# Kernel optimization log

Hardware: AMD Instinct MI355X
Metric: run time of the kernel (lower is better)

Reference implementation:

```python
import jax, jax.numpy as jnp
import numpy as np

B, S, D, H = 2, 2048, 2048, 16
HD = D // H  # 128


def setup_inputs() -> dict:
    key = jax.random.key(0)
    ks = jax.random.split(key, 5)
    x = jax.random.normal(ks[0], (B, S, D), dtype=jnp.float32)
    scale = 1.0 / np.sqrt(D)
    wq = jax.random.normal(ks[1], (D, D), dtype=jnp.float32) * scale
    wk = jax.random.normal(ks[2], (D, D), dtype=jnp.float32) * scale
    wv = jax.random.normal(ks[3], (D, D), dtype=jnp.float32) * scale
    wo = jax.random.normal(ks[4], (D, D), dtype=jnp.float32) * scale
    # RoPE frequencies: theta = 10000, freqs_cis[t, j] = exp(i * t / theta^(2j/HD))
    inv_freq = 1.0 / (10000.0 ** (jnp.arange(0, HD, 2, dtype=jnp.float32) / HD))  # [HD/2]
    t = jnp.arange(S, dtype=jnp.float32)
    ang = jnp.outer(t, inv_freq)  # [S, HD/2]
    freqs_cos = jnp.cos(ang)
    freqs_sin = jnp.sin(ang)
    # Additive causal mask [S, S]
    neg = jnp.float32(-1e9)
    mask = jnp.triu(jnp.full((S, S), neg, dtype=jnp.float32), k=1)
    return {"x": x, "wq": wq, "wk": wk, "wv": wv, "wo": wo,
            "freqs_cos": freqs_cos, "freqs_sin": freqs_sin,
            "mask": mask, "start_pos": 0}


def _rope(t, cos, sin):
    # t: [B, S, H, HD]; cos/sin: [S, HD/2] broadcast as [1, S, 1, HD/2]
    tr = t.reshape(t.shape[:-1] + (HD // 2, 2))
    xr, xi = tr[..., 0], tr[..., 1]
    c = cos[None, :, None, :]
    s = sin[None, :, None, :]
    out_r = xr * c - xi * s
    out_i = xr * s + xi * c
    return jnp.stack([out_r, out_i], axis=-1).reshape(t.shape)


def reference(x, wq, wk, wv, wo, freqs_cos, freqs_sin, mask, start_pos):
    bsz, seqlen, _ = x.shape
    # nn.Linear: y = x @ W.T
    xq = jnp.einsum('bsd,ed->bse', x, wq).reshape(bsz, seqlen, H, HD)
    xk = jnp.einsum('bsd,ed->bse', x, wk).reshape(bsz, seqlen, H, HD)
    xv = jnp.einsum('bsd,ed->bse', x, wv).reshape(bsz, seqlen, H, HD)
    xq = _rope(xq, freqs_cos, freqs_sin)
    xk = _rope(xk, freqs_cos, freqs_sin)
    # [B, H, S, HD]
    xq = xq.transpose(0, 2, 1, 3)
    xk = xk.transpose(0, 2, 1, 3)
    xv = xv.transpose(0, 2, 1, 3)
    scores = jnp.einsum('bhqd,bhkd->bhqk', xq, xk) / jnp.sqrt(jnp.float32(HD))
    scores = scores + mask[None, None, :, :]
    probs = jax.nn.softmax(scores.astype(jnp.float32), axis=-1).astype(xq.dtype)
    out = jnp.einsum('bhqk,bhkd->bhqd', probs, xv)
    out = out.transpose(0, 2, 1, 3).reshape(bsz, seqlen, H * HD)
    return jnp.einsum('bse,de->bsd', out, wo)
```

## Files before the change

### kernel.cpp

```cpp
#include <hip/hip_runtime.h>


#define SQ 2048
#define DQ 2048
#define HQ 16
#define HDQ 128

typedef short bf16x8 __attribute__((ext_vector_type(8)));
typedef short bf16x4 __attribute__((ext_vector_type(4)));
typedef float f32x4 __attribute__((ext_vector_type(4)));

#define WAITVM4 asm volatile("s_waitcnt vmcnt(4)" ::: "memory")
#define WAITVM3 asm volatile("s_waitcnt vmcnt(3)" ::: "memory")
#define WAITVM2 asm volatile("s_waitcnt vmcnt(2)" ::: "memory")
#define WAITVM0 asm volatile("s_waitcnt vmcnt(0)" ::: "memory")

__device__ __forceinline__ short f2bf(float f) {
  union { float f; unsigned u; } v; v.f = f;
  unsigned r = (v.u + 0x7FFFu + ((v.u >> 16) & 1u)) >> 16;
  return (short)r;
}
__device__ __forceinline__ float bf2f(short b) {
  union { unsigned u; float f; } v; v.u = ((unsigned)(unsigned short)b) << 16;
  return v.f;
}
__device__ __forceinline__ void gload_lds16(const void* g, void* l) {
  __builtin_amdgcn_global_load_lds(
      (const __attribute__((address_space(1))) void*)g,
      (__attribute__((address_space(3))) void*)l, 16, 0, 0);
}

__global__ void cvt_kernel(const float* __restrict__ in, short* __restrict__ out, int nvec) {
  int i = blockIdx.x * blockDim.x + threadIdx.x;
  if (i >= nvec) return;
  const f32x4* p = (const f32x4*)in + (size_t)i * 2;
  f32x4 a = p[0], b = p[1];
  bf16x8 o;
  o[0] = f2bf(a[0]); o[1] = f2bf(a[1]); o[2] = f2bf(a[2]); o[3] = f2bf(a[3]);
  o[4] = f2bf(b[0]); o[5] = f2bf(b[1]); o[6] = f2bf(b[2]); o[7] = f2bf(b[3]);
  *((bf16x8*)out + i) = o;
}

__global__ void rope_kernel(short* __restrict__ t, const float* __restrict__ cosT,
                            const float* __restrict__ sinT, float scale, int nvec) {
  int i = blockIdx.x * blockDim.x + threadIdx.x;
  if (i >= nvec) return;
  size_t off = (size_t)i * 8;
  int hd0 = (int)(off & 127);
  int s = (int)((off >> 7) & 2047);
  bf16x8 v = *((const bf16x8*)(t + off));
  f32x4 c  = *(const f32x4*)(cosT + (size_t)s * 64 + (hd0 >> 1));
  f32x4 sn = *(const f32x4*)(sinT + (size_t)s * 64 + (hd0 >> 1));
  bf16x8 o;
#pragma unroll
  for (int p = 0; p < 4; ++p) {
    float xr = bf2f(v[2 * p]), xi = bf2f(v[2 * p + 1]);
    o[2 * p]     = f2bf((xr * c[p] - xi * sn[p]) * scale);
    o[2 * p + 1] = f2bf((xr * sn[p] + xi * c[p]) * scale);
  }
  *((bf16x8*)(t + off)) = o;
}

__global__ void vtrans_kernel(const short* __restrict__ vb, short* __restrict__ vtb) {
  __shared__ __align__(16) short tile[64][72];
  int bh = blockIdx.z, s0 = blockIdx.y * 64, d0 = blockIdx.x * 64;
  int tid = threadIdx.x;
#pragma unroll
  for (int it = 0; it < 2; ++it) {
    int vi = it * 256 + tid;
    int r = vi >> 3, c8 = (vi & 7) * 8;
    bf16x8 v = *(const bf16x8*)&vb[((size_t)bh * SQ + s0 + r) * HDQ + d0 + c8];
    *(bf16x8*)&tile[r][c8] = v;
  }
  __syncthreads();
#pragma unroll
  for (int it = 0; it < 2; ++it) {
    int vi = it * 256 + tid;
    int d = vi >> 3, s8 = (vi & 7) * 8;
    bf16x8 o;
#pragma unroll
    for (int j = 0; j < 8; ++j) o[j] = tile[s8 + j][d];
    *(bf16x8*)&vtb[((size_t)bh * HDQ + d0 + d) * SQ + s0 + s8] = o;
  }
}

template <int BN, int MODE>
__global__ __launch_bounds__(512, 4) void gemmT(const short* __restrict__ A,
                                                const short* __restrict__ W,
                                                short* __restrict__ oQ, short* __restrict__ oK,
                                                short* __restrict__ oV, float* __restrict__ oF) {
  constexpr int NFR = BN / 64;
  constexpr int NIB = BN / 16;
  constexpr int NBX = (MODE == 0) ? (6144 / BN) : (2048 / BN);
  __shared__ __align__(16) short As[3][128 * 32];
  __shared__ __align__(16) short Bs[3][BN * 32];
  const int K = DQ;
  const int NT = K / 32;
  int nwg = gridDim.x, cpx = nwg >> 3;
  int swz = (blockIdx.x & 7) * cpx + (blockIdx.x >> 3);
  int bx = swz % NBX, by = swz / NBX;
  int m0 = by * 128, n0 = bx * BN;
  int tid = threadIdx.x, wid = tid >> 6, lane = tid & 63;
  int wr = wid >> 2, wc = wid & 3;
  f32x4 acc[4][NFR] = {};

  auto stageA = [&](int kt, int buf) {
    int g = wid * 64 + lane;
    int r = g >> 2, q = g & 3;
    gload_lds16(A + (size_t)(m0 + r) * K + kt * 32 + ((q ^ (((r >> 3) & 1) << 1)) * 8),
                &As[buf][wid * 512]);
  };
  auto stageB = [&](int kt, int buf) {
#pragma unroll
    for (int i = wid; i < NIB; i += 8) {
      int g = i * 64 + lane;
      int r = g >> 2, q = g & 3;
      gload_lds16(W + (size_t)(n0 + r) * K + kt * 32 + ((q ^ (((r >> 3) & 1) << 1)) * 8),
                  &Bs[buf][i * 512]);
    }
  };

  stageA(0, 0); stageB(0, 0);
  stageA(1, 1); stageB(1, 1);
  if (BN == 192 && wid < 4) { WAITVM3; } else { WAITVM2; }
  __builtin_amdgcn_s_barrier();

  int cc = (lane >> 4) * 8;
  int cur = 0, nbuf = 2;
#pragma unroll 1
  for (int t = 0; t < NT; ++t) {
    bool st = (t + 2) < NT;
    bf16x8 bfr[NFR], af[4];
#pragma unroll
    for (int nf = 0; nf < NFR; ++nf) {
      int br = wc * (BN / 4) + nf * 16 + (lane & 15);
      bfr[nf] = *(const bf16x8*)&Bs[cur][br * 32 + (cc ^ (((br >> 3) & 1) << 4))];
    }
#pragma unroll
    for (int i = 0; i < 4; ++i) {
      int fr = wr * 64 + i * 16 + (lane & 15);
      af[i] = *(const bf16x8*)&As[cur][fr * 32 + (cc ^ (((fr >> 3) & 1) << 4))];
    }
    if (st) { stageA(t + 2, nbuf); stageB(t + 2, nbuf); }
    __builtin_amdgcn_s_setprio(1);
#pragma unroll
    for (int i = 0; i < 4; ++i)
#pragma unroll
      for (int nf = 0; nf < NFR; ++nf)
        acc[i][nf] = __builtin_amdgcn_mfma_f32_16x16x32_bf16(af[i], bfr[nf], acc[i][nf], 0, 0, 0);
    __builtin_amdgcn_s_setprio(0);
    if (st) {
      if (BN == 192 && wid < 4) { WAITVM3; } else { WAITVM2; }
    } else {
      WAITVM0;
    }
    __builtin_amdgcn_s_barrier();
    cur = (cur == 2) ? 0 : cur + 1;
    nbuf = (nbuf == 2) ? 0 : nbuf + 1;
  }
#pragma unroll
  for (int mf = 0; mf < 4; ++mf) {
    int mb = m0 + wr * 64 + mf * 16 + (lane >> 4) * 4;
#pragma unroll
    for (int nf = 0; nf < NFR; ++nf) {
      int n_lin = n0 + wc * (BN / 4) + nf * 16 + (lane & 15);
#pragma unroll
      for (int j = 0; j < 4; ++j) {
        int m = mb + j;
        float v = acc[mf][nf][j];
        if (MODE == 0) {
          int zsel = n_lin >> 11, col = n_lin & 2047;
          short* oT = (zsel == 0) ? oQ : (zsel == 1) ? oK : oV;
          int b = m >> 11, s = m & 2047, h = col >> 7, hd = col & 127;
          oT[(((size_t)(b * HQ + h)) * SQ + s) * HDQ + hd] = f2bf(v);
        } else {
          oF[(size_t)m * DQ + n_lin] = v;
        }
      }
    }
  }
}

__device__ __forceinline__ void stage_kv32(const short* kbase, const short* vbase, int k0,
                                           short* KsB, short* VtB, int w, int lane) {
#pragma unroll
  for (int i = 0; i < 2; ++i) {
    int c = i * 4 + w;
    int ch = c * 64 + lane;
    int r = ch >> 4, c8 = (ch & 15) * 8;
    gload_lds16(kbase + (size_t)(k0 + r) * HDQ + (c8 ^ ((r & 7) << 3)), KsB + c * 512);
    int d = ch >> 2, k8 = (ch & 3) * 8;
    gload_lds16(vbase + (size_t)d * SQ + k0 + (k8 ^ (((d >> 1) & 3) << 3)), VtB + c * 512);
  }
}

__global__ __launch_bounds__(256, 4) void flash_kernel(const short* __restrict__ qb,
                                                       const short* __restrict__ kb,
                                                       const short* __restrict__ vtb,
                                                       short* __restrict__ ab) {
  __shared__ __align__(16) short Ks[2][32 * 128];
  __shared__ __align__(16) short Vt[2][128 * 32];
  __shared__ __align__(16) short Pl[4][16 * 32];
  int x = blockIdx.x, bh = blockIdx.y;
  int qt = (bh & 8) ? (31 - x) : x;
  int q0 = qt * 64;
  int tid = threadIdx.x, w = tid >> 6, lane = tid & 63;
  int g = lane >> 4, qcol = lane & 15;
  int qw0 = q0 + w * 16;
  const short* qbase = qb + (size_t)bh * SQ * HDQ;
  const short* kbase = kb + (size_t)bh * SQ * HDQ;
  const short* vbase = vtb + (size_t)bh * HDQ * SQ;
  int b = bh >> 4, h = bh & 15;

  bf16x8 qf[4];
#pragma unroll
  for (int ccq = 0; ccq < 4; ++ccq)
    qf[ccq] = *(const bf16x8*)&qbase[(size_t)(qw0 + qcol) * HDQ + ccq * 32 + g * 8];

  f32x4 oacc[8] = {};
  float m_st = -1e30f, l_st = 0.f;
  int nt = 2 * qt + 2;
  stage_kv32(kbase, vbase, 0, Ks[0], Vt[0], w, lane);
#pragma unroll 1
  for (int t = 0; t < nt; ++t) {
    int cur = t & 1;
    int k0 = t * 32;
    __builtin_amdgcn_s_barrier();
    if (t + 1 < nt) {
      stage_kv32(kbase, vbase, (t + 1) * 32, Ks[cur ^ 1], Vt[cur ^ 1], w, lane);
      WAITVM4;
    } else {
      WAITVM0;
    }
    __builtin_amdgcn_s_barrier();
    if (k0 > qw0 + 15) continue;
    f32x4 sacc[2] = {};
    __builtin_amdgcn_s_setprio(1);
#pragma unroll
    for (int nf = 0; nf < 2; ++nf) {
      int rk = nf * 16 + qcol;
#pragma unroll
      for (int ccq = 0; ccq < 4; ++ccq) {
        int ck = ccq * 32 + g * 8;
        bf16x8 kf = *(const bf16x8*)&Ks[cur][rk * 128 + (ck ^ ((rk & 7) << 3))];
        sacc[nf] = __builtin_amdgcn_mfma_f32_16x16x32_bf16(kf, qf[ccq], sacc[nf], 0, 0, 0);
      }
    }
    __builtin_amdgcn_s_setprio(0);
    int q = qw0 + qcol;
    if (k0 + 31 > qw0) {
#pragma unroll
      for (int nf = 0; nf < 2; ++nf)
#pragma unroll
        for (int j = 0; j < 4; ++j) {
          int k = k0 + nf * 16 + g * 4 + j;
          if (k > q) sacc[nf][j] = -1e9f;
        }
    }
    float mt = fmaxf(fmaxf(fmaxf(sacc[0][0], sacc[0][1]), fmaxf(sacc[0][2], sacc[0][3])),
                     fmaxf(fmaxf(sacc[1][0], sacc[1][1]), fmaxf(sacc[1][2], sacc[1][3])));
    mt = fmaxf(mt, __shfl_xor(mt, 16));
    mt = fmaxf(mt, __shfl_xor(mt, 32));
    float mn = fmaxf(m_st, mt);
    float al = exp2f(m_st - mn);
    float p0[4], p1[4];
    float ls = 0.f;
#pragma unroll
    for (int j = 0; j < 4; ++j) { p0[j] = exp2f(sacc[0][j] - mn); ls += p0[j]; }
#pragma unroll
    for (int j = 0; j < 4; ++j) { p1[j] = exp2f(sacc[1][j] - mn); ls += p1[j]; }
    l_st = l_st * al + ls;
    m_st = mn;
    int sw = (qcol & 3) * 8;
    {
      bf16x4 pk;
      pk[0] = f2bf(p0[0]); pk[1] = f2bf(p0[1]); pk[2] = f2bf(p0[2]); pk[3] = f2bf(p0[3]);
      *(bf16x4*)&Pl[w][qcol * 32 + ((g * 4) ^ sw)] = pk;
      pk[0] = f2bf(p1[0]); pk[1] = f2bf(p1[1]); pk[2] = f2bf(p1[2]); pk[3] = f2bf(p1[3]);
      *(bf16x4*)&Pl[w][qcol * 32 + ((16 + g * 4) ^ sw)] = pk;
    }
    f32x4 alv;
    alv[0] = __shfl(al, g * 4 + 0);
    alv[1] = __shfl(al, g * 4 + 1);
    alv[2] = __shfl(al, g * 4 + 2);
    alv[3] = __shfl(al, g * 4 + 3);
#pragma unroll
    for (int df = 0; df < 8; ++df) oacc[df] *= alv;
    bf16x8 pf = *(const bf16x8*)&Pl[w][qcol * 32 + ((g * 8) ^ sw)];
    __builtin_amdgcn_s_setprio(1);
#pragma unroll
    for (int df = 0; df < 8; ++df) {
      int rd = df * 16 + qcol;
      bf16x8 vf = *(const bf16x8*)&Vt[cur][rd * 32 + ((g * 8) ^ (((rd >> 1) & 3) << 3))];
      oacc[df] = __builtin_amdgcn_mfma_f32_16x16x32_bf16(pf, vf, oacc[df], 0, 0, 0);
    }
    __builtin_amdgcn_s_setprio(0);
  }
  l_st += __shfl_xor(l_st, 16);
  l_st += __shfl_xor(l_st, 32);
  float inv = 1.0f / l_st;
  f32x4 invv;
  invv[0] = __shfl(inv, g * 4 + 0);
  invv[1] = __shfl(inv, g * 4 + 1);
  invv[2] = __shfl(inv, g * 4 + 2);
  invv[3] = __shfl(inv, g * 4 + 3);
#pragma unroll
  for (int df = 0; df < 8; ++df)
#pragma unroll
    for (int j = 0; j < 4; ++j) {
      int qq = qw0 + g * 4 + j;
      int dd = df * 16 + qcol;
      ab[((size_t)b * SQ + qq) * DQ + h * HDQ + dd] = f2bf(oacc[df][j] * invv[j]);
    }
}

extern "C" void kernel_launch(void* const* d_in, const int* in_sizes, int n_in,
                              void* d_out, int out_size, void* d_ws, size_t ws_size,
                              hipStream_t stream) {
  (void)in_sizes; (void)n_in; (void)out_size; (void)ws_size;
  const float* x  = (const float*)d_in[0];
  const float* wq = (const float*)d_in[1];
  const float* wk = (const float*)d_in[2];
  const float* wv = (const float*)d_in[3];
  const float* wo = (const float*)d_in[4];
  const float* fc = (const float*)d_in[5];
  const float* fs = (const float*)d_in[6];
  float* out = (float*)d_out;

  short* xb  = (short*)d_ws;
  short* wqb = xb + (size_t)8388608;
  short* wkb = wqb + (size_t)4194304;
  short* wvb = wkb + (size_t)4194304;
  short* wob = wvb + (size_t)4194304;
  short* qb  = wob + (size_t)4194304;
  short* kb  = qb + (size_t)8388608;
  short* ab  = kb + (size_t)8388608;
  short* vb  = (short*)d_out;
  short* vtb = vb + (size_t)8388608;

  cvt_kernel<<<4096, 256, 0, stream>>>(x, xb, 1048576);
  cvt_kernel<<<2048, 256, 0, stream>>>(wq, wqb, 524288);
  cvt_kernel<<<2048, 256, 0, stream>>>(wk, wkb, 524288);
  cvt_kernel<<<2048, 256, 0, stream>>>(wv, wvb, 524288);
  cvt_kernel<<<2048, 256, 0, stream>>>(wo, wob, 524288);

  gemmT<192, 0><<<dim3(1024), 512, 0, stream>>>(xb, wqb, qb, kb, vb, nullptr);

  rope_kernel<<<4096, 256, 0, stream>>>(qb, fc, fs, 0.12751744779976827f, 1048576);
  rope_kernel<<<4096, 256, 0, stream>>>(kb, fc, fs, 1.0f, 1048576);

  vtrans_kernel<<<dim3(2, 32, 32), 256, 0, stream>>>(vb, vtb);

  flash_kernel<<<dim3(32, 32), 256, 0, stream>>>(qb, kb, vtb, ab);

  gemmT<128, 1><<<dim3(512), 512, 0, stream>>>(ab, wob, nullptr, nullptr, nullptr, out);
}
```

Measured before the change: 293.9 us.

## Fuse RoPE and V transpose into QKV GEMM epilogue, merge conversion kernels

```diff
diff --git a/kernel.cpp b/kernel.cpp
--- a/kernel.cpp
+++ b/kernel.cpp
@@ -11,7 +11,6 @@
 typedef float f32x4 __attribute__((ext_vector_type(4)));
 
 #define WAITVM4 asm volatile("s_waitcnt vmcnt(4)" ::: "memory")
-#define WAITVM3 asm volatile("s_waitcnt vmcnt(3)" ::: "memory")
 #define WAITVM2 asm volatile("s_waitcnt vmcnt(2)" ::: "memory")
 #define WAITVM0 asm volatile("s_waitcnt vmcnt(0)" ::: "memory")
 
@@ -30,65 +29,39 @@
       (__attribute__((address_space(3))) void*)l, 16, 0, 0);
 }
 
-__global__ void cvt_kernel(const float* __restrict__ in, short* __restrict__ out, int nvec) {
-  int i = blockIdx.x * blockDim.x + threadIdx.x;
-  if (i >= nvec) return;
-  const f32x4* p = (const f32x4*)in + (size_t)i * 2;
+__global__ void cvt5_kernel(const float* __restrict__ x, const float* __restrict__ wq,
+                            const float* __restrict__ wk, const float* __restrict__ wv,
+                            const float* __restrict__ wo, short* __restrict__ xb,
+                            short* __restrict__ wqb, short* __restrict__ wkb,
+                            short* __restrict__ wvb, short* __restrict__ wob) {
+  int bi = blockIdx.x;
+  const float* src;
+  short* dst;
+  int off;
+  if (bi < 4096) {
+    src = x; dst = xb; off = bi;
+  } else {
+    int t = bi - 4096, wsel = t >> 11;
+    off = t & 2047;
+    src = (wsel == 0) ? wq : (wsel == 1) ? wk : (wsel == 2) ? wv : wo;
+    dst = (wsel == 0) ? wqb : (wsel == 1) ? wkb : (wsel == 2) ? wvb : wob;
+  }
+  int i = off * 256 + threadIdx.x;
+  const f32x4* p = (const f32x4*)src + (size_t)i * 2;
   f32x4 a = p[0], b = p[1];
   bf16x8 o;
   o[0] = f2bf(a[0]); o[1] = f2bf(a[1]); o[2] = f2bf(a[2]); o[3] = f2bf(a[3]);
   o[4] = f2bf(b[0]); o[5] = f2bf(b[1]); o[6] = f2bf(b[2]); o[7] = f2bf(b[3]);
-  *((bf16x8*)out + i) = o;
-}
-
-__global__ void rope_kernel(short* __restrict__ t, const float* __restrict__ cosT,
-                            const float* __restrict__ sinT, float scale, int nvec) {
-  int i = blockIdx.x * blockDim.x + threadIdx.x;
-  if (i >= nvec) return;
-  size_t off = (size_t)i * 8;
-  int hd0 = (int)(off & 127);
-  int s = (int)((off >> 7) & 2047);
-  bf16x8 v = *((const bf16x8*)(t + off));
-  f32x4 c  = *(const f32x4*)(cosT + (size_t)s * 64 + (hd0 >> 1));
-  f32x4 sn = *(const f32x4*)(sinT + (size_t)s * 64 + (hd0 >> 1));
-  bf16x8 o;
-#pragma unroll
-  for (int p = 0; p < 4; ++p) {
-    float xr = bf2f(v[2 * p]), xi = bf2f(v[2 * p + 1]);
-    o[2 * p]     = f2bf((xr * c[p] - xi * sn[p]) * scale);
-    o[2 * p + 1] = f2bf((xr * sn[p] + xi * c[p]) * scale);
-  }
-  *((bf16x8*)(t + off)) = o;
-}
-
-__global__ void vtrans_kernel(const short* __restrict__ vb, short* __restrict__ vtb) {
-  __shared__ __align__(16) short tile[64][72];
-  int bh = blockIdx.z, s0 = blockIdx.y * 64, d0 = blockIdx.x * 64;
-  int tid = threadIdx.x;
-#pragma unroll
-  for (int it = 0; it < 2; ++it) {
-    int vi = it * 256 + tid;
-    int r = vi >> 3, c8 = (vi & 7) * 8;
-    bf16x8 v = *(const bf16x8*)&vb[((size_t)bh * SQ + s0 + r) * HDQ + d0 + c8];
-    *(bf16x8*)&tile[r][c8] = v;
-  }
-  __syncthreads();
-#pragma unroll
-  for (int it = 0; it < 2; ++it) {
-    int vi = it * 256 + tid;
-    int d = vi >> 3, s8 = (vi & 7) * 8;
-    bf16x8 o;
-#pragma unroll
-    for (int j = 0; j < 8; ++j) o[j] = tile[s8 + j][d];
-    *(bf16x8*)&vtb[((size_t)bh * HDQ + d0 + d) * SQ + s0 + s8] = o;
-  }
+  *((bf16x8*)dst + i) = o;
 }
 
 template <int BN, int MODE>
 __global__ __launch_bounds__(512, 4) void gemmT(const short* __restrict__ A,
                                                 const short* __restrict__ W,
                                                 short* __restrict__ oQ, short* __restrict__ oK,
-                                                short* __restrict__ oV, float* __restrict__ oF) {
+                                                short* __restrict__ oV, float* __restrict__ oF,
+                                                const float* __restrict__ cosT,
+                                                const float* __restrict__ sinT) {
   constexpr int NFR = BN / 64;
   constexpr int NIB = BN / 16;
   constexpr int NBX = (MODE == 0) ? (6144 / BN) : (2048 / BN);
@@ -122,7 +95,7 @@
 
   stageA(0, 0); stageB(0, 0);
   stageA(1, 1); stageB(1, 1);
-  if (BN == 192 && wid < 4) { WAITVM3; } else { WAITVM2; }
+  WAITVM2;
   __builtin_amdgcn_s_barrier();
 
   int cc = (lane >> 4) * 8;
@@ -149,11 +122,7 @@
       for (int nf = 0; nf < NFR; ++nf)
         acc[i][nf] = __builtin_amdgcn_mfma_f32_16x16x32_bf16(af[i], bfr[nf], acc[i][nf], 0, 0, 0);
     __builtin_amdgcn_s_setprio(0);
-    if (st) {
-      if (BN == 192 && wid < 4) { WAITVM3; } else { WAITVM2; }
-    } else {
-      WAITVM0;
-    }
+    if (st) { WAITVM2; } else { WAITVM0; }
     __builtin_amdgcn_s_barrier();
     cur = (cur == 2) ? 0 : cur + 1;
     nbuf = (nbuf == 2) ? 0 : nbuf + 1;
@@ -164,17 +133,36 @@
 #pragma unroll
     for (int nf = 0; nf < NFR; ++nf) {
       int n_lin = n0 + wc * (BN / 4) + nf * 16 + (lane & 15);
-#pragma unroll
-      for (int j = 0; j < 4; ++j) {
-        int m = mb + j;
-        float v = acc[mf][nf][j];
-        if (MODE == 0) {
-          int zsel = n_lin >> 11, col = n_lin & 2047;
-          short* oT = (zsel == 0) ? oQ : (zsel == 1) ? oK : oV;
-          int b = m >> 11, s = m & 2047, h = col >> 7, hd = col & 127;
-          oT[(((size_t)(b * HQ + h)) * SQ + s) * HDQ + hd] = f2bf(v);
-        } else {
-          oF[(size_t)m * DQ + n_lin] = v;
+      if (MODE == 1) {
+#pragma unroll
+        for (int j = 0; j < 4; ++j)
+          oF[(size_t)(mb + j) * DQ + n_lin] = acc[mf][nf][j];
+      } else {
+        int zsel = n_lin >> 11, col = n_lin & 2047;
+        int h = col >> 7, hd = col & 127, ii = hd >> 1;
+        float sgn = (hd & 1) ? 1.f : -1.f;
+        float scl = (zsel == 0) ? 0.12751744779976827f : 1.f;
+        float ov[4];
+#pragma unroll
+        for (int j = 0; j < 4; ++j) {
+          int m = mb + j;
+          int s = m & 2047, b = m >> 11;
+          float v = acc[mf][nf][j];
+          float vp = __shfl_xor(v, 1);
+          if (zsel < 2) {
+            float c = cosT[s * 64 + ii], sn = sinT[s * 64 + ii];
+            float o = (v * c + sgn * vp * sn) * scl;
+            short* oT = zsel ? oK : oQ;
+            oT[(((size_t)(b * HQ + h)) * SQ + s) * HDQ + hd] = f2bf(o);
+          } else {
+            ov[j] = v;
+          }
+        }
+        if (zsel == 2) {
+          int b = mb >> 11, s = mb & 2047;
+          bf16x4 pk;
+          pk[0] = f2bf(ov[0]); pk[1] = f2bf(ov[1]); pk[2] = f2bf(ov[2]); pk[3] = f2bf(ov[3]);
+          *(bf16x4*)&oV[(((size_t)(b * HQ + h)) * HDQ + hd) * SQ + s] = pk;
         }
       }
     }
@@ -335,23 +323,14 @@
   short* qb  = wob + (size_t)4194304;
   short* kb  = qb + (size_t)8388608;
   short* ab  = kb + (size_t)8388608;
-  short* vb  = (short*)d_out;
-  short* vtb = vb + (size_t)8388608;
-
-  cvt_kernel<<<4096, 256, 0, stream>>>(x, xb, 1048576);
-  cvt_kernel<<<2048, 256, 0, stream>>>(wq, wqb, 524288);
-  cvt_kernel<<<2048, 256, 0, stream>>>(wk, wkb, 524288);
-  cvt_kernel<<<2048, 256, 0, stream>>>(wv, wvb, 524288);
-  cvt_kernel<<<2048, 256, 0, stream>>>(wo, wob, 524288);
-
-  gemmT<192, 0><<<dim3(1024), 512, 0, stream>>>(xb, wqb, qb, kb, vb, nullptr);
-
-  rope_kernel<<<4096, 256, 0, stream>>>(qb, fc, fs, 0.12751744779976827f, 1048576);
-  rope_kernel<<<4096, 256, 0, stream>>>(kb, fc, fs, 1.0f, 1048576);
-
-  vtrans_kernel<<<dim3(2, 32, 32), 256, 0, stream>>>(vb, vtb);
+  short* vtb = (short*)d_out + (size_t)8388608;
+
+  cvt5_kernel<<<12288, 256, 0, stream>>>(x, wq, wk, wv, wo, xb, wqb, wkb, wvb, wob);
+
+  gemmT<128, 0><<<dim3(1536), 512, 0, stream>>>(xb, wqb, qb, kb, vtb, nullptr, fc, fs);
 
   flash_kernel<<<dim3(32, 32), 256, 0, stream>>>(qb, kb, vtb, ab);
 
-  gemmT<128, 1><<<dim3(512), 512, 0, stream>>>(ab, wob, nullptr, nullptr, nullptr, out);
-}
+  gemmT<128, 1><<<dim3(512), 512, 0, stream>>>(ab, wob, nullptr, nullptr, nullptr, out,
+                                               nullptr, nullptr);
+}
```

Measured after the change: 298.3 us. No clear change (+1.5%).
